# Kernel tuning notes

Hardware: AMD Instinct MI355X
Metric: run time of the kernel (lower is better)

## Reference

```python
import jax, jax.numpy as jnp
import numpy as np
from jax import lax
import math

B, C, H, W, HEADS = 4, 64, 48, 48, 4
CH = C * HEADS
EPS_IN = 1e-5   # InstanceNorm2d eps
EPS_LN = 1e-5   # LayerNorm eps
EPS_NRM = 1e-12 # F.normalize eps


def setup_inputs() -> dict:
    key = jax.random.key(0)
    ks = jax.random.split(key, 8)
    rn = lambda k, shape, s: (jax.random.normal(k, shape, jnp.float32) * s)
    return {
        "emb_all": jax.random.normal(ks[0], (B, C, H, W), jnp.float32),
        "ln_w": jnp.ones((C,), jnp.float32),
        "ln_b": jnp.zeros((C,), jnp.float32),
        "wq": rn(ks[1], (CH, C), 0.05),
        "wk": rn(ks[2], (CH, C), 0.05),
        "wv": rn(ks[3], (CH, C), 0.05),
        "dwq": rn(ks[4], (CH, 1, 3, 3), 0.1),
        "dwk": rn(ks[5], (CH, 1, 3, 3), 0.1),
        "dwv": rn(ks[6], (CH, 1, 3, 3), 0.1),
        "proj_w": rn(ks[7], (C, C), 0.05),
        "proj_b": jnp.zeros((C,), jnp.float32),
    }


def _layernorm_c(x, w, b):
    # Restormer-style 'WithBias' LayerNorm over channel dim of NCHW
    mu = jnp.mean(x, axis=1, keepdims=True)
    var = jnp.mean((x - mu) ** 2, axis=1, keepdims=True)
    xn = (x - mu) / jnp.sqrt(var + EPS_LN)
    return xn * w[None, :, None, None] + b[None, :, None, None]


def _dwconv3(x, k):
    # depthwise 3x3, padding=1, NCHW / OIHW
    return lax.conv_general_dilated(
        x, k, window_strides=(1, 1), padding="SAME",
        feature_group_count=CH,
        dimension_numbers=("NCHW", "OIHW", "NCHW"))


def _qkv_branch(x, w1x1, dw):
    y = jnp.einsum("bchw,oc->bohw", x, w1x1)          # 1x1 conv, no bias
    y = _dwconv3(y, dw)                                # depthwise 3x3
    # b (head c) h w -> b head (h w) c
    y = y.reshape(B, HEADS, C, H * W).transpose(0, 1, 3, 2)
    return y


def reference(emb_all, ln_w, ln_b, wq, wk, wv, dwq, dwk, dwv, proj_w, proj_b):
    org = emb_all
    x = _layernorm_c(emb_all, ln_w, ln_b)

    q = _qkv_branch(x, wq, dwq)   # (B, HEADS, HW, C)
    k = _qkv_branch(x, wk, dwk)
    v = _qkv_branch(x, wv, dwv)

    # L2-normalize along channel dim (F.normalize semantics)
    q = q / jnp.maximum(jnp.linalg.norm(q, axis=-1, keepdims=True), EPS_NRM)
    k = k / jnp.maximum(jnp.linalg.norm(k, axis=-1, keepdims=True), EPS_NRM)

    num = H * W
    atten = jnp.einsum("bhnc,bhmc->bhnm", q, k) / math.sqrt(num)

    # InstanceNorm2d over the (hw x hw) score map, per (batch, head), no affine
    mu = jnp.mean(atten, axis=(-2, -1), keepdims=True)
    var = jnp.mean((atten - mu) ** 2, axis=(-2, -1), keepdims=True)
    atten = (atten - mu) / jnp.sqrt(var + EPS_IN)

    probs = jax.nn.softmax(atten, axis=-1)

    out = jnp.einsum("bhnm,bhmc->bhnc", probs, v)      # (B, HEADS, HW, C)
    out = out.mean(axis=1)                             # average over heads
    out = out.transpose(0, 2, 1).reshape(B, C, H, W)   # b (h w) c -> b c h w
    out = jnp.einsum("bchw,oc->bohw", out, proj_w) + proj_b[None, :, None, None]
    return org + out
```

## Files before the change

kernel.cpp:

```cpp
#include <hip/hip_runtime.h>
#include <hip/hip_bf16.h>
#include <math.h>

#define NB 4
#define NC 64
#define NH 48
#define NW 48
#define NHEADS 4
#define NCH 256
#define NHW 2304
#define NBH 16
#define NCHK 4
#define CHUNK 576
#define NT (CHUNK / 32)

#define OB_Y    0ull
#define OB_GP   0ull
#define OB_SQP  4718592ull
#define OB_OHP  0ull
#define OB_Q    18874368ull
#define OB_K    23592960ull
#define OB_V    28311552ull
#define OB_L    33030144ull
#define OB_SS   33619968ull
#define OB_SA   33620480ull

typedef __bf16 bf16x8 __attribute__((ext_vector_type(8)));
typedef float f32x4 __attribute__((ext_vector_type(4)));
typedef float f32x16 __attribute__((ext_vector_type(16)));

__device__ __forceinline__ float bf2f(ushort u) {
  return __uint_as_float(((unsigned)u) << 16);
}
__device__ __forceinline__ ushort f2bf(float f) {
  __hip_bfloat16 h = __float2bfloat16(f);
  return *(ushort*)&h;
}
__device__ __forceinline__ void gload16(const void* g, void* l) {
  __builtin_amdgcn_global_load_lds((const __attribute__((address_space(1))) unsigned int*)g,
                                   (__attribute__((address_space(3))) unsigned int*)l, 16, 0, 0);
}

__global__ __launch_bounds__(256) void k_lnconv(const float* __restrict__ emb,
                                                const float* __restrict__ lw,
                                                const float* __restrict__ lb,
                                                const float* __restrict__ wq,
                                                const float* __restrict__ wk,
                                                const float* __restrict__ wv,
                                                ushort* __restrict__ Y) {
  __shared__ float Xs[64][68];
  __shared__ float sp[4][64], ssp[4][64];
  __shared__ float mu_s[64], rs_s[64], lw_s[64], lb_s[64];
  int p0 = blockIdx.x * 64, b = blockIdx.y, qkv = blockIdx.z;
  const float* Wm = qkv == 0 ? wq : (qkv == 1 ? wk : wv);
  const float* src = emb + (size_t)b * NC * NHW + p0;
  int t = threadIdx.x;
  for (int e = t; e < 1024; e += 256) {
    int c = e >> 4, p4 = (e & 15) * 4;
    float4 v = *(const float4*)&src[c * NHW + p4];
    Xs[p4][c] = v.x; Xs[p4 + 1][c] = v.y; Xs[p4 + 2][c] = v.z; Xs[p4 + 3][c] = v.w;
  }
  if (t < 64) { lw_s[t] = lw[t]; lb_s[t] = lb[t]; }
  __syncthreads();
  {
    int px = t & 63, cq = t >> 6;
    float s = 0.f, ss = 0.f;
#pragma unroll
    for (int cc = 0; cc < 16; cc += 4) {
      float4 v = *(const float4*)&Xs[px][cq * 16 + cc];
      s += (v.x + v.y) + (v.z + v.w);
      ss += (v.x * v.x + v.y * v.y) + (v.z * v.z + v.w * v.w);
    }
    sp[cq][px] = s;
    ssp[cq][px] = ss;
  }
  __syncthreads();
  if (t < 64) {
    float s4 = (sp[0][t] + sp[1][t]) + (sp[2][t] + sp[3][t]);
    float ss4 = (ssp[0][t] + ssp[1][t]) + (ssp[2][t] + ssp[3][t]);
    float m = s4 * (1.f / 64.f), va = ss4 * (1.f / 64.f) - m * m;
    mu_s[t] = m;
    rs_s[t] = rsqrtf(va + 1e-5f);
  }
  __syncthreads();
  int lane = t & 63, wvi = t >> 6, ql = lane & 31, h = lane >> 5;
  bf16x8 bfr[2][4];
#pragma unroll
  for (int pb = 0; pb < 2; ++pb) {
    int px = pb * 32 + ql;
    float mu = mu_s[px], rs = rs_s[px];
#pragma unroll
    for (int kc = 0; kc < 4; ++kc) {
      union { bf16x8 v; ushort u[8]; } pk;
#pragma unroll
      for (int j = 0; j < 8; ++j) {
        int c = kc * 16 + h * 8 + j;
        pk.u[j] = f2bf((Xs[px][c] - mu) * rs * lw_s[c] + lb_s[c]);
      }
      bfr[pb][kc] = pk.v;
    }
  }
  bf16x8 afr[2][4];
#pragma unroll
  for (int ob = 0; ob < 2; ++ob) {
    const float* wr = Wm + (size_t)(wvi * 64 + ob * 32 + ql) * 64;
#pragma unroll
    for (int kc = 0; kc < 4; ++kc) {
      float4 w0 = *(const float4*)&wr[kc * 16 + h * 8];
      float4 w1 = *(const float4*)&wr[kc * 16 + h * 8 + 4];
      union { bf16x8 v; ushort u[8]; } pk;
      pk.u[0] = f2bf(w0.x); pk.u[1] = f2bf(w0.y); pk.u[2] = f2bf(w0.z); pk.u[3] = f2bf(w0.w);
      pk.u[4] = f2bf(w1.x); pk.u[5] = f2bf(w1.y); pk.u[6] = f2bf(w1.z); pk.u[7] = f2bf(w1.w);
      afr[ob][kc] = pk.v;
    }
  }
  f32x16 d00 = {}, d01 = {}, d10 = {}, d11 = {};
#pragma unroll
  for (int kc = 0; kc < 4; ++kc) {
    d00 = __builtin_amdgcn_mfma_f32_32x32x16_bf16(afr[0][kc], bfr[0][kc], d00, 0, 0, 0);
    d01 = __builtin_amdgcn_mfma_f32_32x32x16_bf16(afr[0][kc], bfr[1][kc], d01, 0, 0, 0);
    d10 = __builtin_amdgcn_mfma_f32_32x32x16_bf16(afr[1][kc], bfr[0][kc], d10, 0, 0, 0);
    d11 = __builtin_amdgcn_mfma_f32_32x32x16_bf16(afr[1][kc], bfr[1][kc], d11, 0, 0, 0);
  }
  ushort* dst = Y + ((size_t)(qkv * NB + b) * NCH + wvi * 64) * NHW + p0;
#pragma unroll
  for (int r = 0; r < 16; ++r) {
    int row = (r & 3) + 8 * (r >> 2) + 4 * h;
    dst[(size_t)row * NHW + ql] = f2bf(d00[r]);
    dst[(size_t)row * NHW + 32 + ql] = f2bf(d01[r]);
    dst[(size_t)(32 + row) * NHW + ql] = f2bf(d10[r]);
    dst[(size_t)(32 + row) * NHW + 32 + ql] = f2bf(d11[r]);
  }
}

__global__ __launch_bounds__(256) void k_dw(const ushort* __restrict__ Y,
                                            const float* __restrict__ dwq,
                                            const float* __restrict__ dwk,
                                            const float* __restrict__ dwv,
                                            ushort* __restrict__ Qo,
                                            ushort* __restrict__ Ko,
                                            ushort* __restrict__ Vo) {
  __shared__ ushort Ys[64][3][48];
  __shared__ float Zs[64][50];
  __shared__ float Ks9[64][9];
  __shared__ float Rp[4][48];
  __shared__ float Rs[48];
  int h = blockIdx.x;
  int hd = blockIdx.y & 3, qkv = blockIdx.y >> 2;
  int b = blockIdx.z;
  int bh = b * NHEADS + hd;
  const float* dwp = qkv == 0 ? dwq : (qkv == 1 ? dwk : dwv);
  const ushort* src = Y + ((size_t)(qkv * NB + b) * NCH + hd * 64) * NHW;
  int t = threadIdx.x;
  for (int e = t; e < 576; e += 256) Ks9[e / 9][e % 9] = dwp[(size_t)hd * 576 + e];
  for (int e = t; e < 2304; e += 256) {
    int c = e / 36, rem = e % 36, r = rem / 12, w4 = (rem % 12) * 4;
    int hh = h + r - 1;
    ushort4 v = (hh >= 0 && hh < NH) ? *(const ushort4*)&src[c * NHW + hh * NW + w4]
                                     : make_ushort4(0, 0, 0, 0);
    *(ushort4*)&Ys[c][r][w4] = v;
  }
  __syncthreads();
  for (int e = t; e < 768; e += 256) {
    int c = e / 12, w4 = (e % 12) * 4;
    float acc0 = 0.f, acc1 = 0.f, acc2 = 0.f, acc3 = 0.f;
#pragma unroll
    for (int r = 0; r < 3; ++r) {
      const ushort* row = &Ys[c][r][0];
      int li = w4 >= 4 ? w4 - 4 : 0;
      int ri = w4 <= 40 ? w4 + 4 : 40;
      uint2 L = *(const uint2*)&row[li];
      uint2 M = *(const uint2*)&row[w4];
      uint2 R = *(const uint2*)&row[ri];
      float vm1 = (w4 == 0) ? 0.f : __uint_as_float(L.y & 0xffff0000u);
      float m0 = __uint_as_float(M.x << 16);
      float m1 = __uint_as_float(M.x & 0xffff0000u);
      float m2 = __uint_as_float(M.y << 16);
      float m3 = __uint_as_float(M.y & 0xffff0000u);
      float v4 = (w4 == 44) ? 0.f : __uint_as_float(R.x << 16);
      float k0 = Ks9[c][r * 3], k1 = Ks9[c][r * 3 + 1], k2 = Ks9[c][r * 3 + 2];
      acc0 += vm1 * k0 + m0 * k1 + m1 * k2;
      acc1 += m0 * k0 + m1 * k1 + m2 * k2;
      acc2 += m1 * k0 + m2 * k1 + m3 * k2;
      acc3 += m2 * k0 + m3 * k1 + v4 * k2;
    }
    *(float2*)&Zs[c][w4] = make_float2(acc0, acc1);
    *(float2*)&Zs[c][w4 + 2] = make_float2(acc2, acc3);
  }
  __syncthreads();
  if (qkv < 2) {
    if (t < 192) {
      int cq = t / 48, w = t % 48;
      float ss = 0.f;
#pragma unroll
      for (int i = 0; i < 16; ++i) { float z = Zs[cq * 16 + i][w]; ss += z * z; }
      Rp[cq][w] = ss;
    }
    __syncthreads();
    if (t < 48)
      Rs[t] = 1.f / fmaxf(sqrtf(Rp[0][t] + Rp[1][t] + Rp[2][t] + Rp[3][t]), 1e-12f);
    __syncthreads();
    ushort* dst = (qkv == 0 ? Qo : Ko) + (size_t)bh * NHW * 64;
    for (int e = t; e < 768; e += 256) {
      int w = e >> 4, c4 = (e & 15) * 4;
      float rsc = Rs[w];
      ushort4 u = make_ushort4(f2bf(Zs[c4][w] * rsc), f2bf(Zs[c4 + 1][w] * rsc),
                               f2bf(Zs[c4 + 2][w] * rsc), f2bf(Zs[c4 + 3][w] * rsc));
      *(ushort4*)&dst[((size_t)(c4 >> 3) * NHW + h * NW + w) * 8 + (c4 & 7)] = u;
    }
  } else {
    ushort* dst = Vo + (size_t)bh * NHW * 64;
    for (int e = t; e < 768; e += 256) {
      int c = e / 12, w4 = (e % 12) * 4;
      float4 z = *(const float4*)&Zs[c][w4];
      ushort4 u = make_ushort4(f2bf(z.x), f2bf(z.y), f2bf(z.z), f2bf(z.w));
      *(ushort4*)&dst[((size_t)(h * 6 + (w4 >> 3)) * 64 + c) * 8 + (w4 & 7)] = u;
    }
  }
}

__global__ __launch_bounds__(256) void k_gram(const ushort* __restrict__ Q,
                                              const ushort* __restrict__ K,
                                              float* __restrict__ Gp,
                                              float* __restrict__ SQp) {
  __shared__ ushort Xt[64][72];
  int ns = blockIdx.x, qk = blockIdx.y, bh = blockIdx.z;
  const ushort* src = (qk ? K : Q) + (size_t)bh * NHW * 64;
  int t = threadIdx.x, lane = t & 63, wv = t >> 6;
  int lr = lane & 15, lg = lane >> 4;
  int ci0 = (wv >> 1) * 32, cj0 = (wv & 1) * 32;
  f32x4 acc[2][2];
#pragma unroll
  for (int i = 0; i < 2; ++i)
#pragma unroll
    for (int j = 0; j < 2; ++j) acc[i][j] = (f32x4){0.f, 0.f, 0.f, 0.f};
  float sq = 0.f;
  for (int it = 0; it < 4; ++it) {
    __syncthreads();
#pragma unroll
    for (int i2 = 0; i2 < 2; ++i2) {
      int n = t & 63, cg = (t >> 6) + 4 * i2;
      union { bf16x8 v; ushort u[8]; } ld;
      ld.v = *(const bf16x8*)&src[((size_t)cg * NHW + ns * 256 + it * 64 + n) * 8];
#pragma unroll
      for (int j = 0; j < 8; ++j) Xt[cg * 8 + j][n] = ld.u[j];
    }
    __syncthreads();
    if (t < 64) {
#pragma unroll
      for (int g = 0; g < 8; ++g) {
        union { bf16x8 v; ushort u[8]; } rd;
        rd.v = *(const bf16x8*)&Xt[t][g * 8];
#pragma unroll
        for (int j = 0; j < 8; ++j) sq += bf2f(rd.u[j]);
      }
    }
#pragma unroll
    for (int kh = 0; kh < 2; ++kh) {
      bf16x8 a0 = *(const bf16x8*)&Xt[ci0 + lr][kh * 32 + lg * 8];
      bf16x8 a1 = *(const bf16x8*)&Xt[ci0 + 16 + lr][kh * 32 + lg * 8];
      bf16x8 b0 = *(const bf16x8*)&Xt[cj0 + lr][kh * 32 + lg * 8];
      bf16x8 b1 = *(const bf16x8*)&Xt[cj0 + 16 + lr][kh * 32 + lg * 8];
      acc[0][0] = __builtin_amdgcn_mfma_f32_16x16x32_bf16(a0, b0, acc[0][0], 0, 0, 0);
      acc[0][1] = __builtin_amdgcn_mfma_f32_16x16x32_bf16(a0, b1, acc[0][1], 0, 0, 0);
      acc[1][0] = __builtin_amdgcn_mfma_f32_16x16x32_bf16(a1, b0, acc[1][0], 0, 0, 0);
      acc[1][1] = __builtin_amdgcn_mfma_f32_16x16x32_bf16(a1, b1, acc[1][1], 0, 0, 0);
    }
  }
  float* g = Gp + ((size_t)(ns * 2 + qk) * NBH + bh) * 4096;
#pragma unroll
  for (int ii = 0; ii < 2; ++ii)
#pragma unroll
    for (int jj = 0; jj < 2; ++jj)
#pragma unroll
      for (int r = 0; r < 4; ++r)
        g[(ci0 + ii * 16 + lg * 4 + r) * 64 + cj0 + jj * 16 + lr] = acc[ii][jj][r];
  if (t < 64) SQp[((size_t)(ns * 2 + qk) * NBH + bh) * 64 + t] = sq;
}

__global__ __launch_bounds__(256) void k_scalep(const float* __restrict__ Gp,
                                                const float* __restrict__ SQp,
                                                float* __restrict__ SSp,
                                                float* __restrict__ SA) {
  __shared__ float red[256];
  int s = blockIdx.x, bh = blockIdx.y, t = threadIdx.x;
  int i0 = s * 512 + t * 2;
  float gq0 = 0.f, gq1 = 0.f, gk0 = 0.f, gk1 = 0.f;
#pragma unroll
  for (int ns = 0; ns < 9; ++ns) {
    float2 q = *(const float2*)&Gp[((size_t)(ns * 2 + 0) * NBH + bh) * 4096 + i0];
    float2 k = *(const float2*)&Gp[((size_t)(ns * 2 + 1) * NBH + bh) * 4096 + i0];
    gq0 += q.x; gq1 += q.y; gk0 += k.x; gk1 += k.y;
  }
  red[t] = gq0 * gk0 + gq1 * gk1;
  __syncthreads();
  if (t < 128) red[t] += red[t + 128];
  __syncthreads();
  if (t < 64) {
    float v = red[t] + red[t + 64];
#pragma unroll
    for (int m = 32; m; m >>= 1) v += __shfl_xor(v, m);
    if (t == 0) SSp[s * NBH + bh] = v;
  }
  if (s == 0 && t < 64) {
    float sq_q = 0.f, sq_k = 0.f;
#pragma unroll
    for (int ns = 0; ns < 9; ++ns) {
      sq_q += SQp[((size_t)(ns * 2 + 0) * NBH + bh) * 64 + t];
      sq_k += SQp[((size_t)(ns * 2 + 1) * NBH + bh) * 64 + t];
    }
    float v2 = sq_q * sq_k;
#pragma unroll
    for (int m = 32; m; m >>= 1) v2 += __shfl_xor(v2, m);
    if (t == 0) SA[bh] = v2;
  }
}

__global__ __launch_bounds__(256, 2) void k_attn(const ushort* __restrict__ Q,
                                                 const ushort* __restrict__ K,
                                                 const ushort* __restrict__ V,
                                                 const float* __restrict__ SSp,
                                                 const float* __restrict__ SA,
                                                 ushort* __restrict__ OHp,
                                                 float* __restrict__ Lp) {
  __shared__ ushort Kl[4][2048];
  __shared__ ushort Vl[4][2048];
  int p = blockIdx.x;
  int gb = p & 7;
  int w = p >> 3;
  int qt = w % 18;
  int rem = w / 18;
  int chunk = rem & 3;
  int bh = gb * 2 + (rem >> 2);
  int t = threadIdx.x, lane = t & 63, wv = t >> 6;
  int ql = lane & 31, h = lane >> 5;
  int q0 = qt * 128 + wv * 32;
  int m00 = chunk * CHUNK;
  const ushort* base = Q + (size_t)bh * NHW * 64;

  float ssf = 0.f;
#pragma unroll
  for (int s = 0; s < 8; ++s) ssf += SSp[s * NBH + bh];
  float saf = SA[bh];
  const double N2 = (double)NHW * (double)NHW;
  double mean = (double)saf / (N2 * 48.0);
  double ea2 = (double)ssf / (N2 * 2304.0);
  double var = ea2 - mean * mean;
  float sc2 = (float)((1.0 / sqrt(var + 1e-5)) / 48.0 * 1.4426950408889634);

  bf16x8 qfr[4];
#pragma unroll
  for (int kc = 0; kc < 4; ++kc)
    qfr[kc] = *(const bf16x8*)&base[((size_t)(kc * 2 + h) * NHW + q0 + ql) * 8];
  asm volatile("s_waitcnt vmcnt(0)" ::: "memory");

  const ushort* kst = K + (size_t)bh * NHW * 64 + ((size_t)(wv * 2 + h) * NHW + m00 + ql) * 8;
  const ushort* vst = V + (size_t)bh * NHW * 64 + ((size_t)((m00 >> 3) + wv) * 64 + lane) * 8;

  f32x16 o0 = {}, o1 = {};
  float lp = 0.f;

  auto COMPUTE = [&](int cb) {
    bf16x8 ka[4], vb[4];
#pragma unroll
    for (int i = 0; i < 4; ++i)
      ka[i] = *(const bf16x8*)&Kl[cb][(2 * i + h) * 256 + ql * 8];
    vb[0] = *(const bf16x8*)&Vl[cb][h * 512 + ql * 8];
    vb[1] = *(const bf16x8*)&Vl[cb][(2 + h) * 512 + ql * 8];
    vb[2] = *(const bf16x8*)&Vl[cb][h * 512 + (ql + 32) * 8];
    vb[3] = *(const bf16x8*)&Vl[cb][(2 + h) * 512 + (ql + 32) * 8];
    __builtin_amdgcn_s_setprio(1);
    f32x16 s = {};
    s = __builtin_amdgcn_mfma_f32_32x32x16_bf16(ka[0], qfr[0], s, 0, 0, 0);
    s = __builtin_amdgcn_mfma_f32_32x32x16_bf16(ka[1], qfr[1], s, 0, 0, 0);
    s = __builtin_amdgcn_mfma_f32_32x32x16_bf16(ka[2], qfr[2], s, 0, 0, 0);
    s = __builtin_amdgcn_mfma_f32_32x32x16_bf16(ka[3], qfr[3], s, 0, 0, 0);
    __builtin_amdgcn_s_setprio(0);
    float pv[16];
    float l0 = 0.f, l1 = 0.f, l2 = 0.f, l3 = 0.f;
#pragma unroll
    for (int r = 0; r < 16; r += 4) {
      pv[r] = __builtin_exp2f(s[r] * sc2);
      pv[r + 1] = __builtin_exp2f(s[r + 1] * sc2);
      pv[r + 2] = __builtin_exp2f(s[r + 2] * sc2);
      pv[r + 3] = __builtin_exp2f(s[r + 3] * sc2);
      l0 += pv[r]; l1 += pv[r + 1]; l2 += pv[r + 2]; l3 += pv[r + 3];
    }
    lp += (l0 + l1) + (l2 + l3);
    uint u[8];
#pragma unroll
    for (int i = 0; i < 8; ++i)
      asm("v_cvt_pk_bf16_f32 %0, %1, %2" : "=v"(u[i]) : "v"(pv[2 * i]), "v"(pv[2 * i + 1]));
    asm volatile("v_permlane32_swap_b32 %0, %1" : "+v"(u[0]), "+v"(u[2]));
    asm volatile("v_permlane32_swap_b32 %0, %1" : "+v"(u[1]), "+v"(u[3]));
    asm volatile("v_permlane32_swap_b32 %0, %1" : "+v"(u[4]), "+v"(u[6]));
    asm volatile("v_permlane32_swap_b32 %0, %1" : "+v"(u[5]), "+v"(u[7]));
    union { uint uu[4]; bf16x8 v; } pa0, pa1;
    pa0.uu[0] = u[0]; pa0.uu[1] = u[1]; pa0.uu[2] = u[2]; pa0.uu[3] = u[3];
    pa1.uu[0] = u[4]; pa1.uu[1] = u[5]; pa1.uu[2] = u[6]; pa1.uu[3] = u[7];
    __builtin_amdgcn_s_setprio(1);
    o0 = __builtin_amdgcn_mfma_f32_32x32x16_bf16(pa0.v, vb[0], o0, 0, 0, 0);
    o0 = __builtin_amdgcn_mfma_f32_32x32x16_bf16(pa1.v, vb[1], o0, 0, 0, 0);
    o1 = __builtin_amdgcn_mfma_f32_32x32x16_bf16(pa0.v, vb[2], o1, 0, 0, 0);
    o1 = __builtin_amdgcn_mfma_f32_32x32x16_bf16(pa1.v, vb[3], o1, 0, 0, 0);
    __builtin_amdgcn_s_setprio(0);
  };

  gload16(kst, (void*)&Kl[0][wv * 512]);
  gload16(vst, (void*)&Vl[0][wv * 512]);
  gload16(kst + 256, (void*)&Kl[1][wv * 512]);
  gload16(vst + 2048, (void*)&Vl[1][wv * 512]);

  for (int mt = 0; mt < NT - 2; ++mt) {
    int sb = (mt + 2) & 3;
    gload16(kst + (size_t)(mt + 2) * 256, (void*)&Kl[sb][wv * 512]);
    gload16(vst + (size_t)(mt + 2) * 2048, (void*)&Vl[sb][wv * 512]);
    asm volatile("s_waitcnt vmcnt(4)" ::: "memory");
    __builtin_amdgcn_s_barrier();
    COMPUTE(mt & 3);
  }
  asm volatile("s_waitcnt vmcnt(2)" ::: "memory");
  __builtin_amdgcn_s_barrier();
  COMPUTE((NT - 2) & 3);
  asm volatile("s_waitcnt vmcnt(0)" ::: "memory");
  __builtin_amdgcn_s_barrier();
  COMPUTE((NT - 1) & 3);

  lp += __shfl_xor(lp, 32);
  if (h == 0) Lp[(size_t)(chunk * NBH + bh) * NHW + q0 + ql] = lp;
  ushort* od = OHp + ((size_t)(chunk * NBH + bh) * NHW + q0) * 64;
#pragma unroll
  for (int r = 0; r < 16; ++r) {
    int qrow = (r & 3) + 8 * (r >> 2) + 4 * h;
    od[(size_t)qrow * 64 + ql] = f2bf(o0[r]);
    od[(size_t)qrow * 64 + 32 + ql] = f2bf(o1[r]);
  }
}

__global__ __launch_bounds__(256) void k_proj(const ushort* __restrict__ OHp,
                                              const float* __restrict__ Lp,
                                              const float* __restrict__ PW,
                                              const float* __restrict__ PB,
                                              const float* __restrict__ org,
                                              float* __restrict__ out) {
  __shared__ float Ls[4][4][16];
  __shared__ float linv[4][16];
  __shared__ float Ms[64][17];
  int p0 = blockIdx.x * 16, b = blockIdx.y;
  int t = threadIdx.x;
  {
    int ck = t >> 6, hd = (t >> 4) & 3, p = t & 15;
    Ls[ck][hd][p] = Lp[(size_t)(ck * NBH + b * 4 + hd) * NHW + p0 + p];
  }
  __syncthreads();
  if (t < 64) {
    int hd = t >> 4, p = t & 15;
    linv[hd][p] = 1.f / (Ls[0][hd][p] + Ls[1][hd][p] + Ls[2][hd][p] + Ls[3][hd][p]);
  }
  __syncthreads();
  {
    int p = t >> 4, c4 = (t & 15) * 4;
    float a0 = 0.f, a1 = 0.f, a2 = 0.f, a3 = 0.f;
#pragma unroll
    for (int hd = 0; hd < 4; ++hd) {
      float s0 = 0.f, s1 = 0.f, s2 = 0.f, s3 = 0.f;
#pragma unroll
      for (int ck = 0; ck < 4; ++ck) {
        ushort4 u = *(const ushort4*)&OHp[((size_t)(ck * NBH + b * 4 + hd) * NHW + p0 + p) * 64 + c4];
        s0 += bf2f(u.x); s1 += bf2f(u.y); s2 += bf2f(u.z); s3 += bf2f(u.w);
      }
      float li = linv[hd][p];
      a0 += s0 * li; a1 += s1 * li; a2 += s2 * li; a3 += s3 * li;
    }
    Ms[c4][p] = 0.25f * a0;
    Ms[c4 + 1][p] = 0.25f * a1;
    Ms[c4 + 2][p] = 0.25f * a2;
    Ms[c4 + 3][p] = 0.25f * a3;
  }
  __syncthreads();
  int p = t & 15, og = t >> 4;
  float acc[4];
#pragma unroll
  for (int i = 0; i < 4; ++i) acc[i] = PB[og * 4 + i];
  for (int c = 0; c < 64; ++c) {
    float xr = Ms[c][p];
#pragma unroll
    for (int i = 0; i < 4; ++i) acc[i] += PW[(og * 4 + i) * 64 + c] * xr;
  }
  const float* orgp = org + (size_t)b * NC * NHW + p0 + p;
  float* outp = out + (size_t)b * NC * NHW + p0 + p;
#pragma unroll
  for (int i = 0; i < 4; ++i) {
    int oc = og * 4 + i;
    outp[(size_t)oc * NHW] = orgp[(size_t)oc * NHW] + acc[i];
  }
}

extern "C" void kernel_launch(void* const* d_in, const int* in_sizes, int n_in,
                              void* d_out, int out_size, void* d_ws, size_t ws_size,
                              hipStream_t stream) {
  const float* emb = (const float*)d_in[0];
  const float* lnw = (const float*)d_in[1];
  const float* lnb = (const float*)d_in[2];
  const float* wq  = (const float*)d_in[3];
  const float* wk  = (const float*)d_in[4];
  const float* wv  = (const float*)d_in[5];
  const float* dwq = (const float*)d_in[6];
  const float* dwk = (const float*)d_in[7];
  const float* dwv = (const float*)d_in[8];
  const float* pw  = (const float*)d_in[9];
  const float* pb  = (const float*)d_in[10];
  char* ws = (char*)d_ws;
  ushort* Y   = (ushort*)(ws + OB_Y);
  float*  Gp  = (float*)(ws + OB_GP);
  float*  SQp = (float*)(ws + OB_SQP);
  ushort* OHp = (ushort*)(ws + OB_OHP);
  ushort* Qb  = (ushort*)(ws + OB_Q);
  ushort* Kb  = (ushort*)(ws + OB_K);
  ushort* Vb  = (ushort*)(ws + OB_V);
  float*  Lpt = (float*)(ws + OB_L);
  float*  SSp = (float*)(ws + OB_SS);
  float*  SAp = (float*)(ws + OB_SA);
  float* out = (float*)d_out;

  k_lnconv<<<dim3(NHW / 64, NB, 3), 256, 0, stream>>>(emb, lnw, lnb, wq, wk, wv, Y);
  k_dw<<<dim3(NH, 12, NB), 256, 0, stream>>>(Y, dwq, dwk, dwv, Qb, Kb, Vb);
  k_gram<<<dim3(9, 2, NBH), 256, 0, stream>>>(Qb, Kb, Gp, SQp);
  k_scalep<<<dim3(8, NBH), 256, 0, stream>>>(Gp, SQp, SSp, SAp);
  k_attn<<<dim3(1152), 256, 0, stream>>>(Qb, Kb, Vb, SSp, SAp, OHp, Lpt);
  k_proj<<<dim3(NHW / 16, NB), 256, 0, stream>>>(OHp, Lpt, pw, pb, emb, out);
}
```

Baseline: 102.6 us.

## Fuse LayerNorm and 1x1 conv into depthwise conv kernel

Merges the LayerNorm plus 1x1 projection kernel into the depthwise 3x3 kernel. Each block loads its three input rows, normalizes them in LDS and computes the 64 head channels with MFMA, then runs the depthwise conv in place. This removes the intermediate Y buffer write and read and one kernel launch. In exchange, the 1x1 conv is recomputed for halo rows, roughly three times per output row, and LayerNorm runs on bf16-rounded inputs, which slightly changes numerics.

```diff
diff --git a/kernel.cpp b/kernel.cpp
--- a/kernel.cpp
+++ b/kernel.cpp
@@ -14,7 +14,6 @@
 #define CHUNK 576
 #define NT (CHUNK / 32)
 
-#define OB_Y    0ull
 #define OB_GP   0ull
 #define OB_SQP  4718592ull
 #define OB_OHP  0ull
@@ -41,132 +40,138 @@
                                    (__attribute__((address_space(3))) unsigned int*)l, 16, 0, 0);
 }
 
-__global__ __launch_bounds__(256) void k_lnconv(const float* __restrict__ emb,
-                                                const float* __restrict__ lw,
-                                                const float* __restrict__ lb,
-                                                const float* __restrict__ wq,
-                                                const float* __restrict__ wk,
-                                                const float* __restrict__ wv,
-                                                ushort* __restrict__ Y) {
-  __shared__ float Xs[64][68];
-  __shared__ float sp[4][64], ssp[4][64];
-  __shared__ float mu_s[64], rs_s[64], lw_s[64], lb_s[64];
-  int p0 = blockIdx.x * 64, b = blockIdx.y, qkv = blockIdx.z;
-  const float* Wm = qkv == 0 ? wq : (qkv == 1 ? wk : wv);
-  const float* src = emb + (size_t)b * NC * NHW + p0;
-  int t = threadIdx.x;
-  for (int e = t; e < 1024; e += 256) {
-    int c = e >> 4, p4 = (e & 15) * 4;
-    float4 v = *(const float4*)&src[c * NHW + p4];
-    Xs[p4][c] = v.x; Xs[p4 + 1][c] = v.y; Xs[p4 + 2][c] = v.z; Xs[p4 + 3][c] = v.w;
-  }
-  if (t < 64) { lw_s[t] = lw[t]; lb_s[t] = lb[t]; }
-  __syncthreads();
-  {
-    int px = t & 63, cq = t >> 6;
-    float s = 0.f, ss = 0.f;
-#pragma unroll
-    for (int cc = 0; cc < 16; cc += 4) {
-      float4 v = *(const float4*)&Xs[px][cq * 16 + cc];
-      s += (v.x + v.y) + (v.z + v.w);
-      ss += (v.x * v.x + v.y * v.y) + (v.z * v.z + v.w * v.w);
-    }
-    sp[cq][px] = s;
-    ssp[cq][px] = ss;
-  }
-  __syncthreads();
-  if (t < 64) {
-    float s4 = (sp[0][t] + sp[1][t]) + (sp[2][t] + sp[3][t]);
-    float ss4 = (ssp[0][t] + ssp[1][t]) + (ssp[2][t] + ssp[3][t]);
-    float m = s4 * (1.f / 64.f), va = ss4 * (1.f / 64.f) - m * m;
-    mu_s[t] = m;
-    rs_s[t] = rsqrtf(va + 1e-5f);
-  }
-  __syncthreads();
-  int lane = t & 63, wvi = t >> 6, ql = lane & 31, h = lane >> 5;
-  bf16x8 bfr[2][4];
-#pragma unroll
-  for (int pb = 0; pb < 2; ++pb) {
-    int px = pb * 32 + ql;
-    float mu = mu_s[px], rs = rs_s[px];
-#pragma unroll
-    for (int kc = 0; kc < 4; ++kc) {
-      union { bf16x8 v; ushort u[8]; } pk;
-#pragma unroll
-      for (int j = 0; j < 8; ++j) {
-        int c = kc * 16 + h * 8 + j;
-        pk.u[j] = f2bf((Xs[px][c] - mu) * rs * lw_s[c] + lb_s[c]);
-      }
-      bfr[pb][kc] = pk.v;
-    }
-  }
-  bf16x8 afr[2][4];
-#pragma unroll
-  for (int ob = 0; ob < 2; ++ob) {
-    const float* wr = Wm + (size_t)(wvi * 64 + ob * 32 + ql) * 64;
-#pragma unroll
-    for (int kc = 0; kc < 4; ++kc) {
-      float4 w0 = *(const float4*)&wr[kc * 16 + h * 8];
-      float4 w1 = *(const float4*)&wr[kc * 16 + h * 8 + 4];
-      union { bf16x8 v; ushort u[8]; } pk;
-      pk.u[0] = f2bf(w0.x); pk.u[1] = f2bf(w0.y); pk.u[2] = f2bf(w0.z); pk.u[3] = f2bf(w0.w);
-      pk.u[4] = f2bf(w1.x); pk.u[5] = f2bf(w1.y); pk.u[6] = f2bf(w1.z); pk.u[7] = f2bf(w1.w);
-      afr[ob][kc] = pk.v;
-    }
-  }
-  f32x16 d00 = {}, d01 = {}, d10 = {}, d11 = {};
-#pragma unroll
-  for (int kc = 0; kc < 4; ++kc) {
-    d00 = __builtin_amdgcn_mfma_f32_32x32x16_bf16(afr[0][kc], bfr[0][kc], d00, 0, 0, 0);
-    d01 = __builtin_amdgcn_mfma_f32_32x32x16_bf16(afr[0][kc], bfr[1][kc], d01, 0, 0, 0);
-    d10 = __builtin_amdgcn_mfma_f32_32x32x16_bf16(afr[1][kc], bfr[0][kc], d10, 0, 0, 0);
-    d11 = __builtin_amdgcn_mfma_f32_32x32x16_bf16(afr[1][kc], bfr[1][kc], d11, 0, 0, 0);
-  }
-  ushort* dst = Y + ((size_t)(qkv * NB + b) * NCH + wvi * 64) * NHW + p0;
-#pragma unroll
-  for (int r = 0; r < 16; ++r) {
-    int row = (r & 3) + 8 * (r >> 2) + 4 * h;
-    dst[(size_t)row * NHW + ql] = f2bf(d00[r]);
-    dst[(size_t)row * NHW + 32 + ql] = f2bf(d01[r]);
-    dst[(size_t)(32 + row) * NHW + ql] = f2bf(d10[r]);
-    dst[(size_t)(32 + row) * NHW + 32 + ql] = f2bf(d11[r]);
-  }
-}
-
-__global__ __launch_bounds__(256) void k_dw(const ushort* __restrict__ Y,
-                                            const float* __restrict__ dwq,
-                                            const float* __restrict__ dwk,
-                                            const float* __restrict__ dwv,
-                                            ushort* __restrict__ Qo,
-                                            ushort* __restrict__ Ko,
-                                            ushort* __restrict__ Vo) {
-  __shared__ ushort Ys[64][3][48];
-  __shared__ float Zs[64][50];
-  __shared__ float Ks9[64][9];
-  __shared__ float Rp[4][48];
-  __shared__ float Rs[48];
+#define DF_ZS 20736
+#define DF_K9 33536
+#define DF_RP 35840
+#define DF_RS 36608
+#define DF_MU 36800
+#define DF_RSD 37376
+#define DF_LW 37952
+#define DF_LB 38208
+__global__ __launch_bounds__(256) void k_dwf(const float* __restrict__ emb,
+                                             const float* __restrict__ lw,
+                                             const float* __restrict__ lb,
+                                             const float* __restrict__ wq,
+                                             const float* __restrict__ wk,
+                                             const float* __restrict__ wv,
+                                             const float* __restrict__ dwq,
+                                             const float* __restrict__ dwk,
+                                             const float* __restrict__ dwv,
+                                             ushort* __restrict__ Qo,
+                                             ushort* __restrict__ Ko,
+                                             ushort* __restrict__ Vo) {
+  __shared__ __align__(16) char pool[38464];
+  ushort* Eb = (ushort*)pool;
+  ushort* Yl = (ushort*)pool;
+  float* Zs = (float*)(pool + DF_ZS);
+  float* Ks9 = (float*)(pool + DF_K9);
+  float* Rp = (float*)(pool + DF_RP);
+  float* Rs = (float*)(pool + DF_RS);
+  float* mu_s = (float*)(pool + DF_MU);
+  float* rs_s = (float*)(pool + DF_RSD);
+  float* lw_s = (float*)(pool + DF_LW);
+  float* lb_s = (float*)(pool + DF_LB);
+
   int h = blockIdx.x;
   int hd = blockIdx.y & 3, qkv = blockIdx.y >> 2;
   int b = blockIdx.z;
   int bh = b * NHEADS + hd;
+  const float* Wm = qkv == 0 ? wq : (qkv == 1 ? wk : wv);
   const float* dwp = qkv == 0 ? dwq : (qkv == 1 ? dwk : dwv);
-  const ushort* src = Y + ((size_t)(qkv * NB + b) * NCH + hd * 64) * NHW;
-  int t = threadIdx.x;
-  for (int e = t; e < 576; e += 256) Ks9[e / 9][e % 9] = dwp[(size_t)hd * 576 + e];
+  int t = threadIdx.x, lane = t & 63, wvi = t >> 6;
+  int l15 = lane & 15, l4 = lane >> 4;
+
   for (int e = t; e < 2304; e += 256) {
     int c = e / 36, rem = e % 36, r = rem / 12, w4 = (rem % 12) * 4;
     int hh = h + r - 1;
-    ushort4 v = (hh >= 0 && hh < NH) ? *(const ushort4*)&src[c * NHW + hh * NW + w4]
-                                     : make_ushort4(0, 0, 0, 0);
-    *(ushort4*)&Ys[c][r][w4] = v;
-  }
+    float4 v = (hh >= 0 && hh < NH)
+                   ? *(const float4*)&emb[((size_t)b * NC + c) * NHW + hh * NW + w4]
+                   : make_float4(0.f, 0.f, 0.f, 0.f);
+    int c8 = c >> 3, cl = c & 7;
+    float vv[4] = {v.x, v.y, v.z, v.w};
+#pragma unroll
+    for (int i = 0; i < 4; ++i) {
+      int px = r * 48 + w4 + i;
+      int ch = c8 ^ ((px >> 3) & 7);
+      Eb[px * 72 + ch * 8 + cl] = f2bf(vv[i]);
+    }
+  }
+  if (t < 64) { lw_s[t] = lw[t]; lb_s[t] = lb[t]; }
+  for (int e = t; e < 576; e += 256) Ks9[e] = dwp[(size_t)hd * 576 + e];
+  __syncthreads();
+  if (t < 144) {
+    int xp = (t >> 3) & 7;
+    float s = 0.f, ss = 0.f;
+#pragma unroll
+    for (int c8 = 0; c8 < 8; ++c8) {
+      union { bf16x8 v; ushort u[8]; } rd;
+      rd.v = *(const bf16x8*)&Eb[t * 72 + (c8 ^ xp) * 8];
+#pragma unroll
+      for (int j = 0; j < 8; ++j) { float v = bf2f(rd.u[j]); s += v; ss += v * v; }
+    }
+    float m = s * (1.f / 64.f), va = ss * (1.f / 64.f) - m * m;
+    mu_s[t] = m;
+    rs_s[t] = rsqrtf(va + 1e-5f);
+  }
+  __syncthreads();
+  if (t < 144) {
+    int xp = (t >> 3) & 7;
+    float mu = mu_s[t], rs = rs_s[t];
+#pragma unroll
+    for (int c8 = 0; c8 < 8; ++c8) {
+      ushort* ptr = &Eb[t * 72 + (c8 ^ xp) * 8];
+      union { bf16x8 v; ushort u[8]; } rd;
+      rd.v = *(const bf16x8*)ptr;
+#pragma unroll
+      for (int j = 0; j < 8; ++j) {
+        int c = c8 * 8 + j;
+        rd.u[j] = f2bf((bf2f(rd.u[j]) - mu) * rs * lw_s[c] + lb_s[c]);
+      }
+      *(bf16x8*)ptr = rd.v;
+    }
+  }
+  __syncthreads();
+  f32x4 acc[9];
+#pragma unroll
+  for (int i = 0; i < 9; ++i) acc[i] = (f32x4){0.f, 0.f, 0.f, 0.f};
+  {
+    bf16x8 afr[2];
+    const float* wr = Wm + (size_t)(hd * 64 + wvi * 16 + l15) * 64;
+#pragma unroll
+    for (int kc = 0; kc < 2; ++kc) {
+      float4 w0 = *(const float4*)&wr[kc * 32 + l4 * 8];
+      float4 w1 = *(const float4*)&wr[kc * 32 + l4 * 8 + 4];
+      union { bf16x8 v; ushort u[8]; } pk;
+      pk.u[0] = f2bf(w0.x); pk.u[1] = f2bf(w0.y); pk.u[2] = f2bf(w0.z); pk.u[3] = f2bf(w0.w);
+      pk.u[4] = f2bf(w1.x); pk.u[5] = f2bf(w1.y); pk.u[6] = f2bf(w1.z); pk.u[7] = f2bf(w1.w);
+      afr[kc] = pk.v;
+    }
+#pragma unroll
+    for (int pxt = 0; pxt < 9; ++pxt) {
+      int px = pxt * 16 + l15;
+      int xp = (px >> 3) & 7;
+#pragma unroll
+      for (int kc = 0; kc < 2; ++kc) {
+        int c8 = kc * 4 + l4;
+        bf16x8 bfr = *(const bf16x8*)&Eb[px * 72 + (c8 ^ xp) * 8];
+        acc[pxt] = __builtin_amdgcn_mfma_f32_16x16x32_bf16(afr[kc], bfr, acc[pxt], 0, 0, 0);
+      }
+    }
+  }
+  __syncthreads();
+#pragma unroll
+  for (int pxt = 0; pxt < 9; ++pxt)
+#pragma unroll
+    for (int r = 0; r < 4; ++r)
+      Yl[(wvi * 16 + l4 * 4 + r) * 148 + pxt * 16 + l15] = f2bf(acc[pxt][r]);
   __syncthreads();
   for (int e = t; e < 768; e += 256) {
     int c = e / 12, w4 = (e % 12) * 4;
     float acc0 = 0.f, acc1 = 0.f, acc2 = 0.f, acc3 = 0.f;
 #pragma unroll
     for (int r = 0; r < 3; ++r) {
-      const ushort* row = &Ys[c][r][0];
+      bool rOK = (unsigned)(h + r - 1) < (unsigned)NH;
+      const ushort* row = &Yl[c * 148 + r * 48];
       int li = w4 >= 4 ? w4 - 4 : 0;
       int ri = w4 <= 40 ? w4 + 4 : 40;
       uint2 L = *(const uint2*)&row[li];
@@ -178,14 +183,16 @@
       float m2 = __uint_as_float(M.y << 16);
       float m3 = __uint_as_float(M.y & 0xffff0000u);
       float v4 = (w4 == 44) ? 0.f : __uint_as_float(R.x << 16);
-      float k0 = Ks9[c][r * 3], k1 = Ks9[c][r * 3 + 1], k2 = Ks9[c][r * 3 + 2];
+      float k0 = rOK ? Ks9[c * 9 + r * 3] : 0.f;
+      float k1 = rOK ? Ks9[c * 9 + r * 3 + 1] : 0.f;
+      float k2 = rOK ? Ks9[c * 9 + r * 3 + 2] : 0.f;
       acc0 += vm1 * k0 + m0 * k1 + m1 * k2;
       acc1 += m0 * k0 + m1 * k1 + m2 * k2;
       acc2 += m1 * k0 + m2 * k1 + m3 * k2;
       acc3 += m2 * k0 + m3 * k1 + v4 * k2;
     }
-    *(float2*)&Zs[c][w4] = make_float2(acc0, acc1);
-    *(float2*)&Zs[c][w4 + 2] = make_float2(acc2, acc3);
+    *(float2*)&Zs[c * 50 + w4] = make_float2(acc0, acc1);
+    *(float2*)&Zs[c * 50 + w4 + 2] = make_float2(acc2, acc3);
   }
   __syncthreads();
   if (qkv < 2) {
@@ -193,26 +200,26 @@
       int cq = t / 48, w = t % 48;
       float ss = 0.f;
 #pragma unroll
-      for (int i = 0; i < 16; ++i) { float z = Zs[cq * 16 + i][w]; ss += z * z; }
-      Rp[cq][w] = ss;
+      for (int i = 0; i < 16; ++i) { float z = Zs[(cq * 16 + i) * 50 + w]; ss += z * z; }
+      Rp[cq * 48 + w] = ss;
     }
     __syncthreads();
     if (t < 48)
-      Rs[t] = 1.f / fmaxf(sqrtf(Rp[0][t] + Rp[1][t] + Rp[2][t] + Rp[3][t]), 1e-12f);
+      Rs[t] = 1.f / fmaxf(sqrtf(Rp[t] + Rp[48 + t] + Rp[96 + t] + Rp[144 + t]), 1e-12f);
     __syncthreads();
     ushort* dst = (qkv == 0 ? Qo : Ko) + (size_t)bh * NHW * 64;
     for (int e = t; e < 768; e += 256) {
       int w = e >> 4, c4 = (e & 15) * 4;
       float rsc = Rs[w];
-      ushort4 u = make_ushort4(f2bf(Zs[c4][w] * rsc), f2bf(Zs[c4 + 1][w] * rsc),
-                               f2bf(Zs[c4 + 2][w] * rsc), f2bf(Zs[c4 + 3][w] * rsc));
+      ushort4 u = make_ushort4(f2bf(Zs[c4 * 50 + w] * rsc), f2bf(Zs[(c4 + 1) * 50 + w] * rsc),
+                               f2bf(Zs[(c4 + 2) * 50 + w] * rsc), f2bf(Zs[(c4 + 3) * 50 + w] * rsc));
       *(ushort4*)&dst[((size_t)(c4 >> 3) * NHW + h * NW + w) * 8 + (c4 & 7)] = u;
     }
   } else {
     ushort* dst = Vo + (size_t)bh * NHW * 64;
     for (int e = t; e < 768; e += 256) {
       int c = e / 12, w4 = (e % 12) * 4;
-      float4 z = *(const float4*)&Zs[c][w4];
+      float4 z = *(const float4*)&Zs[c * 50 + w4];
       ushort4 u = make_ushort4(f2bf(z.x), f2bf(z.y), f2bf(z.z), f2bf(z.w));
       *(ushort4*)&dst[((size_t)(h * 6 + (w4 >> 3)) * 64 + c) * 8 + (w4 & 7)] = u;
     }
@@ -511,7 +518,6 @@
   const float* pw  = (const float*)d_in[9];
   const float* pb  = (const float*)d_in[10];
   char* ws = (char*)d_ws;
-  ushort* Y   = (ushort*)(ws + OB_Y);
   float*  Gp  = (float*)(ws + OB_GP);
   float*  SQp = (float*)(ws + OB_SQP);
   ushort* OHp = (ushort*)(ws + OB_OHP);
@@ -523,8 +529,8 @@
   float*  SAp = (float*)(ws + OB_SA);
   float* out = (float*)d_out;
 
-  k_lnconv<<<dim3(NHW / 64, NB, 3), 256, 0, stream>>>(emb, lnw, lnb, wq, wk, wv, Y);
-  k_dw<<<dim3(NH, 12, NB), 256, 0, stream>>>(Y, dwq, dwk, dwv, Qb, Kb, Vb);
+  k_dwf<<<dim3(NH, 12, NB), 256, 0, stream>>>(emb, lnw, lnb, wq, wk, wv, dwq, dwk, dwv,
+                                              Qb, Kb, Vb);
   k_gram<<<dim3(9, 2, NBH), 256, 0, stream>>>(Qb, Kb, Gp, SQp);
   k_scalep<<<dim3(8, NBH), 256, 0, stream>>>(Gp, SQp, SSp, SAp);
   k_attn<<<dim3(1152), 256, 0, stream>>>(Qb, Kb, Vb, SSp, SAp, OHp, Lpt);
```

After: 98.53 us (median of 2 runs). -3.9%, faster.
